# Optimization experiments

Measured on AMD Instinct MI355X. Metric: run time of the kernel, lower is better.

The kernel has to match this reference:

```python
import jax, jax.numpy as jnp
import numpy as np

KERNEL_SIZE = 5
SIGMA = 2.0
HALF_K = KERNEL_SIZE // 2


def _gaussian_kernel():
    # torch: arange(-k//2+1, k//2+1) with python floor div -> [-2,...,2] for k=5
    ax = jnp.arange(-(KERNEL_SIZE // 2), KERNEL_SIZE // 2 + 1, dtype=jnp.float32)
    xx, yy = jnp.meshgrid(ax, ax, indexing='ij')
    k = jnp.exp(-(xx ** 2 + yy ** 2) / (2.0 * SIGMA ** 2))
    return k / k.sum()  # [5,5]


def setup_inputs() -> dict:
    key = jax.random.key(0)
    k1, k2 = jax.random.split(key)
    feature_map = jax.random.normal(k1, (512, 256, 256), dtype=jnp.float32)
    keypoints = jax.random.randint(k2, (4096, 2), 0, 256, dtype=jnp.int64)
    return {"feature_map": feature_map, "keypoints": keypoints}


def reference(feature_map, keypoints):
    C, H, W = feature_map.shape
    kern = _gaussian_kernel().astype(feature_map.dtype)  # [5,5]
    x = jnp.clip(keypoints[:, 0].astype(jnp.int32), HALF_K, W - HALF_K - 1)  # [N]
    y = jnp.clip(keypoints[:, 1].astype(jnp.int32), HALF_K, H - HALF_K - 1)  # [N]

    def pool_one(xi, yi):
        patch = jax.lax.dynamic_slice(
            feature_map, (0, yi - HALF_K, xi - HALF_K), (C, KERNEL_SIZE, KERNEL_SIZE)
        )  # [C,5,5]
        return jnp.einsum('chw,hw->c', patch, kern)  # [C]

    return jax.vmap(pool_one)(x, y)  # [N,C]
```

## Files before the change

kernel.cpp:

```cpp
#include <hip/hip_runtime.h>


#define NC  512
#define NH  256
#define NW  256
#define NKP 4096

#define NSTRIP 8
#define STRIP_SHIFT 5
#define SLICE_ROWS 36
#define STR 260
#define CAPW 192

__global__ __launch_bounds__(256) void pool_kernel(
    const float* __restrict__ fm, const int* __restrict__ kp,
    float* __restrict__ out)
{
    __shared__ float    plane[SLICE_ROWS * STR];
    __shared__ unsigned lds_list[4 * CAPW];
    __shared__ int      cnt[4];

    const int b     = blockIdx.x;
    const int x7    = b & 7;
    const int inner = b >> 3;
    const int hi    = inner >> 7;
    const int rem   = inner & 127;
    const int q     = rem >> 4;
    const int l16   = rem & 15;
    const int chunk = (hi << 3) | x7;
    const int c     = (chunk << 4) | l16;

    const int t    = threadIdx.x;
    const int w    = t >> 6;
    const int lane = t & 63;
    const int ybase = (q << STRIP_SHIFT) - 2;
    const unsigned long long lmlt = (1ull << lane) - 1ull;

    const int4* kp4 = (const int4*)kp;
    int4 vv[8];
#pragma unroll
    for (int it = 0; it < 8; ++it)
        vv[it] = kp4[(w << 9) + (it << 6) + lane];

    const float* src = fm + ((size_t)c << 16);
#pragma unroll
    for (int it = 0; it < 9; ++it) {
        const int row = w + (it << 2);
        const int gr  = ybase + row;
        if ((unsigned)gr < 256u) {
            const float* gp = src + ((size_t)gr << 8) + (lane << 2);
            float*       lp = &plane[row * STR + (lane << 2)];
            __builtin_amdgcn_global_load_lds(
                (const __attribute__((address_space(1))) void*)gp,
                (__attribute__((address_space(3))) void*)lp,
                16, 0, 0);
        }
    }

    int off = 0;
#pragma unroll
    for (int it = 0; it < 8; ++it) {
        const int i0 = (((w << 9) + (it << 6) + lane) << 1);
        {
            const int x = min(max(vv[it].x, 2), NW - 3);
            const int y = min(max(vv[it].y, 2), NH - 3);
            const bool m = ((y >> STRIP_SHIFT) == q);
            const unsigned long long bal = __ballot(m);
            const int pos = off + __popcll(bal & lmlt);
            if (m && pos < CAPW)
                lds_list[w * CAPW + pos] =
                    (unsigned)i0 | ((unsigned)x << 12) | ((unsigned)y << 20);
            off += __popcll(bal);
        }
        {
            const int x = min(max(vv[it].z, 2), NW - 3);
            const int y = min(max(vv[it].w, 2), NH - 3);
            const bool m = ((y >> STRIP_SHIFT) == q);
            const unsigned long long bal = __ballot(m);
            const int pos = off + __popcll(bal & lmlt);
            if (m && pos < CAPW)
                lds_list[w * CAPW + pos] =
                    (unsigned)(i0 + 1) | ((unsigned)x << 12) | ((unsigned)y << 20);
            off += __popcll(bal);
        }
    }
    if (lane == 0) cnt[w] = off;

    const float e1 = 0.8824969025845955f;
    const float e2 = 0.6065306597126334f;
    const float s  = 2.0f * (e1 + e2) + 1.0f;
    const float inv_s2 = 1.0f / (s * s);
    const float g[5] = {e2, e1, 1.0f, e1, e2};
    float gy[5];
#pragma unroll
    for (int i = 0; i < 5; i++) gy[i] = g[i] * inv_s2;

    __syncthreads();

    for (int seg = 0; seg < 4; ++seg) {
        const int cs = min(cnt[seg], CAPW);
        for (int e = t; e < cs; e += 256) {
            const unsigned pk = lds_list[seg * CAPW + e];
            const int n  = (int)(pk & 0xFFFu);
            const int xc = (int)((pk >> 12) & 0xFFu);
            const int yc = (int)((pk >> 20) & 0xFFu);

            const int x0 = xc - 2;
            const int r  = x0 & 3;
            const int xa = x0 - r;
            float wx[8];
#pragma unroll
            for (int i = 0; i < 8; i++)
                wx[i] = (i >= r && i < r + 5) ? g[i - r] : 0.0f;

            const int lr0 = yc - (q << STRIP_SHIFT);
            float acc = 0.0f;
#pragma unroll
            for (int dy = 0; dy < 5; dy++) {
                const float* rowp = &plane[(lr0 + dy) * STR + xa];
                float4 a  = *(const float4*)rowp;
                float4 b4 = *(const float4*)(rowp + 4);
                acc += gy[dy] * (a.x * wx[0] + a.y * wx[1] + a.z * wx[2] + a.w * wx[3]
                               + b4.x * wx[4] + b4.y * wx[5] + b4.z * wx[6] + b4.w * wx[7]);
            }
            out[(size_t)n * NC + c] = acc;
        }
    }

    if (cnt[w] > CAPW) {
        int off2 = 0;
#pragma unroll 1
        for (int it = 0; it < 8; ++it) {
            const int4 v = kp4[(w << 9) + (it << 6) + lane];
            const int i0 = (((w << 9) + (it << 6) + lane) << 1);
#pragma unroll
            for (int half = 0; half < 2; ++half) {
                const int xr = half ? v.z : v.x;
                const int yr = half ? v.w : v.y;
                const int x = min(max(xr, 2), NW - 3);
                const int y = min(max(yr, 2), NH - 3);
                const bool m = ((y >> STRIP_SHIFT) == q);
                const unsigned long long bal = __ballot(m);
                const int pos = off2 + __popcll(bal & lmlt);
                if (m && pos >= CAPW) {
                    const int x0 = x - 2;
                    const int r  = x0 & 3;
                    const int xa = x0 - r;
                    float wx[8];
#pragma unroll
                    for (int i = 0; i < 8; i++)
                        wx[i] = (i >= r && i < r + 5) ? g[i - r] : 0.0f;
                    const int lr0 = y - (q << STRIP_SHIFT);
                    float acc = 0.0f;
#pragma unroll
                    for (int dy = 0; dy < 5; dy++) {
                        const float* rowp = &plane[(lr0 + dy) * STR + xa];
                        float4 a  = *(const float4*)rowp;
                        float4 b4 = *(const float4*)(rowp + 4);
                        acc += gy[dy] * (a.x * wx[0] + a.y * wx[1] + a.z * wx[2] + a.w * wx[3]
                                       + b4.x * wx[4] + b4.y * wx[5] + b4.z * wx[6] + b4.w * wx[7]);
                    }
                    out[(size_t)(i0 + half) * NC + c] = acc;
                }
                off2 += __popcll(bal);
            }
        }
    }
}

__global__ __launch_bounds__(256) void gpool_direct_kernel(
    const float* __restrict__ fm, const int* __restrict__ kp,
    float* __restrict__ out)
{
    const int n = blockIdx.x;
    const int t = threadIdx.x;

    int x = kp[2 * n + 0];
    int y = kp[2 * n + 1];
    x = min(max(x, 2), NW - 3);
    y = min(max(y, 2), NH - 3);

    const float e1 = 0.8824969025845955f;
    const float e2 = 0.6065306597126334f;
    const float s  = 2.0f * (e1 + e2) + 1.0f;
    const float inv_s2 = 1.0f / (s * s);
    float g[5] = {e2, e1, 1.0f, e1, e2};
    float gy[5];
#pragma unroll
    for (int i = 0; i < 5; i++) gy[i] = g[i] * inv_s2;

    const int x0 = x - 2;
    const int r  = x0 & 3;
    const int xa = x0 - r;
    float wx[8];
#pragma unroll
    for (int i = 0; i < 8; i++)
        wx[i] = (i >= r && i < r + 5) ? g[i - r] : 0.0f;

    const float* base0 = fm + ((size_t)t * NH + (y - 2)) * NW + xa;
    const float* base1 = fm + ((size_t)(t + 256) * NH + (y - 2)) * NW + xa;

    float acc0 = 0.0f, acc1 = 0.0f;
#pragma unroll
    for (int dy = 0; dy < 5; dy++) {
        const float4* p0 = (const float4*)(base0 + dy * NW);
        const float4* p1 = (const float4*)(base1 + dy * NW);
        float4 a0 = p0[0], b0 = p0[1], a1 = p1[0], b1 = p1[1];
        acc0 += gy[dy] * (a0.x * wx[0] + a0.y * wx[1] + a0.z * wx[2] + a0.w * wx[3]
                        + b0.x * wx[4] + b0.y * wx[5] + b0.z * wx[6] + b0.w * wx[7]);
        acc1 += gy[dy] * (a1.x * wx[0] + a1.y * wx[1] + a1.z * wx[2] + a1.w * wx[3]
                        + b1.x * wx[4] + b1.y * wx[5] + b1.z * wx[6] + b1.w * wx[7]);
    }

    out[(size_t)n * NC + t]       = acc0;
    out[(size_t)n * NC + t + 256] = acc1;
}

extern "C" void kernel_launch(void* const* d_in, const int* in_sizes, int n_in,
                              void* d_out, int out_size, void* d_ws, size_t ws_size,
                              hipStream_t stream)
{
    const float* fm  = (const float*)d_in[0];
    const int*   kp  = (const int*)d_in[1];
    float*       out = (float*)d_out;
    const int n_kp   = in_sizes[1] / 2;

    (void)d_ws; (void)ws_size;

    if (n_kp == NKP) {
        pool_kernel<<<NC * NSTRIP, 256, 0, stream>>>(fm, kp, out);
    } else {
        gpool_direct_kernel<<<n_kp, 256, 0, stream>>>(fm, kp, out);
    }
}
```

Measured before the change: 199.0 us.

## Process 8 channels per block with double-buffered LDS staging and vectorized stores

Each block now handles a group of 8 channels for one row strip instead of a single channel. The next channel slice is staged into a second LDS buffer while the current one is pooled, and keypoint decoding is done once and reused across the 8 channels. Outputs are written as two float4 stores per keypoint instead of scattered single-float writes, and the keypoint filtering cost is spread over 8 channels. In exchange, LDS use doubles and register pressure rises from the per-channel result arrays. The code also assumes at most 256 keypoints per wave segment, dropping the old strided loop over entries.

```diff
diff --git a/kernel.cpp b/kernel.cpp
--- a/kernel.cpp
+++ b/kernel.cpp
@@ -10,25 +10,28 @@
 #define STRIP_SHIFT 5
 #define SLICE_ROWS 36
 #define STR 260
+#define PLANE (SLICE_ROWS * STR)
 #define CAPW 192
+#define G 8
 
 __global__ __launch_bounds__(256) void pool_kernel(
     const float* __restrict__ fm, const int* __restrict__ kp,
     float* __restrict__ out)
 {
-    __shared__ float    plane[SLICE_ROWS * STR];
+    __shared__ float    plane[2 * PLANE];
     __shared__ unsigned lds_list[4 * CAPW];
     __shared__ int      cnt[4];
 
     const int b     = blockIdx.x;
     const int x7    = b & 7;
     const int inner = b >> 3;
-    const int hi    = inner >> 7;
-    const int rem   = inner & 127;
-    const int q     = rem >> 4;
-    const int l16   = rem & 15;
-    const int chunk = (hi << 3) | x7;
-    const int c     = (chunk << 4) | l16;
+    const int hi    = inner >> 4;
+    const int rem   = inner & 15;
+    const int q     = rem >> 1;
+    const int m     = rem & 1;
+    const int p     = (hi << 3) | x7;
+    const int gidx  = (p << 1) | m;
+    const int c0    = gidx << 3;
 
     const int t    = threadIdx.x;
     const int w    = t >> 6;
@@ -42,20 +45,24 @@
     for (int it = 0; it < 8; ++it)
         vv[it] = kp4[(w << 9) + (it << 6) + lane];
 
-    const float* src = fm + ((size_t)c << 16);
-#pragma unroll
-    for (int it = 0; it < 9; ++it) {
-        const int row = w + (it << 2);
-        const int gr  = ybase + row;
-        if ((unsigned)gr < 256u) {
-            const float* gp = src + ((size_t)gr << 8) + (lane << 2);
-            float*       lp = &plane[row * STR + (lane << 2)];
-            __builtin_amdgcn_global_load_lds(
-                (const __attribute__((address_space(1))) void*)gp,
-                (__attribute__((address_space(3))) void*)lp,
-                16, 0, 0);
-        }
-    }
+#define STAGE(CH, BASE)                                                        \
+    do {                                                                       \
+        const float* _src = fm + ((size_t)(CH) << 16);                         \
+        _Pragma("unroll")                                                      \
+        for (int _k = 0; _k < 9; ++_k) {                                       \
+            const int _row = w + (_k << 2);                                    \
+            const int _gr  = ybase + _row;                                     \
+            if ((unsigned)_gr < 256u) {                                        \
+                const float* _gp = _src + (_gr << 8) + (lane << 2);            \
+                float*       _lp = (BASE) + _row * STR + (lane << 2);          \
+                __builtin_amdgcn_global_load_lds(                              \
+                    (const __attribute__((address_space(1))) void*)_gp,        \
+                    (__attribute__((address_space(3))) void*)_lp, 16, 0, 0);   \
+            }                                                                  \
+        }                                                                      \
+    } while (0)
+
+    STAGE(c0, plane);
 
     int off = 0;
 #pragma unroll
@@ -64,10 +71,10 @@
         {
             const int x = min(max(vv[it].x, 2), NW - 3);
             const int y = min(max(vv[it].y, 2), NH - 3);
-            const bool m = ((y >> STRIP_SHIFT) == q);
-            const unsigned long long bal = __ballot(m);
+            const bool mm = ((y >> STRIP_SHIFT) == q);
+            const unsigned long long bal = __ballot(mm);
             const int pos = off + __popcll(bal & lmlt);
-            if (m && pos < CAPW)
+            if (mm && pos < CAPW)
                 lds_list[w * CAPW + pos] =
                     (unsigned)i0 | ((unsigned)x << 12) | ((unsigned)y << 20);
             off += __popcll(bal);
@@ -75,10 +82,10 @@
         {
             const int x = min(max(vv[it].z, 2), NW - 3);
             const int y = min(max(vv[it].w, 2), NH - 3);
-            const bool m = ((y >> STRIP_SHIFT) == q);
-            const unsigned long long bal = __ballot(m);
+            const bool mm = ((y >> STRIP_SHIFT) == q);
+            const unsigned long long bal = __ballot(mm);
             const int pos = off + __popcll(bal & lmlt);
-            if (m && pos < CAPW)
+            if (mm && pos < CAPW)
                 lds_list[w * CAPW + pos] =
                     (unsigned)(i0 + 1) | ((unsigned)x << 12) | ((unsigned)y << 20);
             off += __popcll(bal);
@@ -95,35 +102,72 @@
 #pragma unroll
     for (int i = 0; i < 5; i++) gy[i] = g[i] * inv_s2;
 
-    __syncthreads();
-
+    bool  ev[4];
+    int   en[4], elr0[4];
+    int   exa[4];
+    float ewx[4][8];
+    float res[4][G];
+
+#pragma unroll
+    for (int i = 0; i < G; ++i) {
+        __syncthreads();
+
+        if (i < G - 1)
+            STAGE(c0 + i + 1, plane + ((i + 1) & 1) * PLANE);
+
+        if (i == 0) {
+#pragma unroll
+            for (int seg = 0; seg < 4; ++seg) {
+                const int cs = min(cnt[seg], CAPW);
+                ev[seg] = (t < cs);
+                en[seg] = 0; exa[seg] = 0; elr0[seg] = 0;
+#pragma unroll
+                for (int j = 0; j < 8; ++j) ewx[seg][j] = 0.0f;
+                if (ev[seg]) {
+                    const unsigned pk = lds_list[seg * CAPW + t];
+                    const int n  = (int)(pk & 0xFFFu);
+                    const int xc = (int)((pk >> 12) & 0xFFu);
+                    const int yc = (int)((pk >> 20) & 0xFFu);
+                    const int x0 = xc - 2;
+                    const int r  = x0 & 3;
+                    en[seg]   = n;
+                    exa[seg]  = x0 - r;
+                    elr0[seg] = yc - (q << STRIP_SHIFT);
+#pragma unroll
+                    for (int j = 0; j < 8; ++j)
+                        ewx[seg][j] = (j >= r && j < r + 5) ? g[j - r] : 0.0f;
+                }
+            }
+        }
+
+        const float* cur = plane + (i & 1) * PLANE;
+#pragma unroll
+        for (int seg = 0; seg < 4; ++seg) {
+            if (ev[seg]) {
+                float acc = 0.0f;
+#pragma unroll
+                for (int dy = 0; dy < 5; ++dy) {
+                    const float* rowp = &cur[(elr0[seg] + dy) * STR + exa[seg]];
+                    float4 a  = *(const float4*)rowp;
+                    float4 b4 = *(const float4*)(rowp + 4);
+                    acc += gy[dy] * (a.x * ewx[seg][0] + a.y * ewx[seg][1]
+                                   + a.z * ewx[seg][2] + a.w * ewx[seg][3]
+                                   + b4.x * ewx[seg][4] + b4.y * ewx[seg][5]
+                                   + b4.z * ewx[seg][6] + b4.w * ewx[seg][7]);
+                }
+                res[seg][i] = acc;
+            }
+        }
+    }
+
+#pragma unroll
     for (int seg = 0; seg < 4; ++seg) {
-        const int cs = min(cnt[seg], CAPW);
-        for (int e = t; e < cs; e += 256) {
-            const unsigned pk = lds_list[seg * CAPW + e];
-            const int n  = (int)(pk & 0xFFFu);
-            const int xc = (int)((pk >> 12) & 0xFFu);
-            const int yc = (int)((pk >> 20) & 0xFFu);
-
-            const int x0 = xc - 2;
-            const int r  = x0 & 3;
-            const int xa = x0 - r;
-            float wx[8];
-#pragma unroll
-            for (int i = 0; i < 8; i++)
-                wx[i] = (i >= r && i < r + 5) ? g[i - r] : 0.0f;
-
-            const int lr0 = yc - (q << STRIP_SHIFT);
-            float acc = 0.0f;
-#pragma unroll
-            for (int dy = 0; dy < 5; dy++) {
-                const float* rowp = &plane[(lr0 + dy) * STR + xa];
-                float4 a  = *(const float4*)rowp;
-                float4 b4 = *(const float4*)(rowp + 4);
-                acc += gy[dy] * (a.x * wx[0] + a.y * wx[1] + a.z * wx[2] + a.w * wx[3]
-                               + b4.x * wx[4] + b4.y * wx[5] + b4.z * wx[6] + b4.w * wx[7]);
-            }
-            out[(size_t)n * NC + c] = acc;
+        if (ev[seg]) {
+            float4 s0 = make_float4(res[seg][0], res[seg][1], res[seg][2], res[seg][3]);
+            float4 s1 = make_float4(res[seg][4], res[seg][5], res[seg][6], res[seg][7]);
+            float* op = out + (size_t)en[seg] * NC + c0;
+            *(float4*)op       = s0;
+            *((float4*)op + 1) = s1;
         }
     }
 
@@ -139,33 +183,38 @@
                 const int yr = half ? v.w : v.y;
                 const int x = min(max(xr, 2), NW - 3);
                 const int y = min(max(yr, 2), NH - 3);
-                const bool m = ((y >> STRIP_SHIFT) == q);
-                const unsigned long long bal = __ballot(m);
+                const bool mm = ((y >> STRIP_SHIFT) == q);
+                const unsigned long long bal = __ballot(mm);
                 const int pos = off2 + __popcll(bal & lmlt);
-                if (m && pos >= CAPW) {
+                if (mm && pos >= CAPW) {
                     const int x0 = x - 2;
                     const int r  = x0 & 3;
                     const int xa = x0 - r;
                     float wx[8];
 #pragma unroll
-                    for (int i = 0; i < 8; i++)
-                        wx[i] = (i >= r && i < r + 5) ? g[i - r] : 0.0f;
-                    const int lr0 = y - (q << STRIP_SHIFT);
-                    float acc = 0.0f;
-#pragma unroll
-                    for (int dy = 0; dy < 5; dy++) {
-                        const float* rowp = &plane[(lr0 + dy) * STR + xa];
-                        float4 a  = *(const float4*)rowp;
-                        float4 b4 = *(const float4*)(rowp + 4);
-                        acc += gy[dy] * (a.x * wx[0] + a.y * wx[1] + a.z * wx[2] + a.w * wx[3]
-                                       + b4.x * wx[4] + b4.y * wx[5] + b4.z * wx[6] + b4.w * wx[7]);
+                    for (int j = 0; j < 8; ++j)
+                        wx[j] = (j >= r && j < r + 5) ? g[j - r] : 0.0f;
+#pragma unroll 1
+                    for (int ch = 0; ch < G; ++ch) {
+                        const float* base = fm + (((size_t)(c0 + ch)) << 16)
+                                          + (size_t)(y - 2) * NW + xa;
+                        float acc = 0.0f;
+#pragma unroll
+                        for (int dy = 0; dy < 5; ++dy) {
+                            const float4* p0 = (const float4*)(base + dy * NW);
+                            float4 a = p0[0], b4 = p0[1];
+                            acc += gy[dy] * (a.x * wx[0] + a.y * wx[1] + a.z * wx[2]
+                                           + a.w * wx[3] + b4.x * wx[4] + b4.y * wx[5]
+                                           + b4.z * wx[6] + b4.w * wx[7]);
+                        }
+                        out[(size_t)(i0 + half) * NC + c0 + ch] = acc;
                     }
-                    out[(size_t)(i0 + half) * NC + c] = acc;
                 }
                 off2 += __popcll(bal);
             }
         }
     }
+#undef STAGE
 }
 
 __global__ __launch_bounds__(256) void gpool_direct_kernel(
@@ -228,7 +277,7 @@
     (void)d_ws; (void)ws_size;
 
     if (n_kp == NKP) {
-        pool_kernel<<<NC * NSTRIP, 256, 0, stream>>>(fm, kp, out);
+        pool_kernel<<<NSTRIP * (NC / G), 256, 0, stream>>>(fm, kp, out);
     } else {
         gpool_direct_kernel<<<n_kp, 256, 0, stream>>>(fm, kp, out);
     }
```

New measurement: 194.2 us. 2.4% less time.
